# Performance work log

Hardware: AMD Instinct MI355X
Metric: run time of the kernel (lower is better)

## Reference

```python
import jax, jax.numpy as jnp
import numpy as np

H = 64
VOCAB = 64
THRESH_SCALE = 0.4
LN_EPS = 1e-5
NORM_EPS = 1e-12


def setup_inputs() -> dict:
    key = jax.random.key(0)
    ks = jax.random.split(key, 16)
    B, L = 64, 1024
    s = 1.0 / np.sqrt(H)
    inp = {
        "seq": jax.random.randint(ks[0], (B, L), 0, VOCAB),
        "embed_W": jax.random.normal(ks[1], (VOCAB, H), jnp.float32),
        "ff_W1": jax.random.normal(ks[2], (H, 2 * H), jnp.float32) * s,
        "ff_b1": jnp.zeros((2 * H,), jnp.float32),
        "ff_W2": jax.random.normal(ks[3], (2 * H, H), jnp.float32) * s,
        "ff_b2": jnp.zeros((H,), jnp.float32),
        "ln_g": jnp.ones((H,), jnp.float32),
        "ln_b": jnp.zeros((H,), jnp.float32),
        "kp_W": jax.random.normal(ks[4], (H, H), jnp.float32) * s,
        "vp_W": jax.random.normal(ks[5], (H, H), jnp.float32) * s,
        "qp_W": jax.random.normal(ks[6], (H, H), jnp.float32) * s,
        "rp_W": jax.random.normal(ks[7], (H, H), jnp.float32) * s,
        "rp_b": jnp.zeros((H,), jnp.float32),
        "out_W": jax.random.normal(ks[8], (H, VOCAB), jnp.float32) * s,
        "out_b": jnp.zeros((VOCAB,), jnp.float32),
    }
    return inp


def _forward(seq, embed_W, ff_W1, ff_b1, ff_W2, ff_b2, ln_g, ln_b,
             kp_W, vp_W, qp_W, rp_W, rp_b, out_W, out_b):
    h = embed_W[seq]                                    # [B, L, H]
    ff = jnp.maximum(h @ ff_W1 + ff_b1, 0.0) @ ff_W2 + ff_b2
    x = h + ff
    mu = x.mean(-1, keepdims=True)
    var = ((x - mu) ** 2).mean(-1, keepdims=True)       # biased var (torch LayerNorm)
    hn = (x - mu) / jnp.sqrt(var + LN_EPS) * ln_g + ln_b
    B, L, _ = hn.shape

    # Precompute all per-step keys/values, then scan the fast-weight update.
    k_all = hn[:, :-1] @ kp_W                           # [B, L-1, H]
    v_all = hn[:, :-1] @ vp_W                           # [B, L-1, H]
    kn_all = k_all / jnp.maximum(
        jnp.linalg.norm(k_all, axis=-1, keepdims=True), NORM_EPS)

    def step(M, kv):
        kn, v = kv                                      # each [B, H]
        vp = jnp.einsum('bij,bj->bi', M, kn)            # read M along k
        err = jnp.linalg.norm(v - vp, axis=-1)          # [B]
        gate = jnp.where(err > THRESH_SCALE * jnp.linalg.norm(v, axis=-1),
                         1.0, 0.0)                      # hard energy gate
        M = M + gate[:, None, None] * jnp.einsum('bi,bj->bij', v - vp, kn)
        return M, None

    M0 = jnp.zeros((B, H, H), dtype=hn.dtype)
    M, _ = jax.lax.scan(step, M0,
                        (kn_all.transpose(1, 0, 2), v_all.transpose(1, 0, 2)))

    q = hn[:, -1] @ qp_W                                # [B, H]
    r = jnp.einsum('bij,bj->bi', M, q) @ rp_W + rp_b
    return r @ out_W + out_b                            # [B, VOCAB]


def reference(seq, embed_W, ff_W1, ff_b1, ff_W2, ff_b2, ln_g, ln_b,
              kp_W, vp_W, qp_W, rp_W, rp_b, out_W, out_b):
    return _forward(seq, embed_W, ff_W1, ff_b1, ff_W2, ff_b2, ln_g, ln_b,
                    kp_W, vp_W, qp_W, rp_W, rp_b, out_W, out_b)
```

## Files before the change

### kernel.cpp

```cpp
#include <hip/hip_runtime.h>
#include <hip/hip_bf16.h>
#include <math.h>

#define BB 64
#define LL 1024
#define HH 64

typedef float v4f __attribute__((ext_vector_type(4)));

__global__ __launch_bounds__(256, 1)
void token_kernel(const int* __restrict__ seq,
                  const float* __restrict__ embed_W,
                  const float* __restrict__ ff_W1, const float* __restrict__ ff_b1,
                  const float* __restrict__ ff_W2, const float* __restrict__ ff_b2,
                  const float* __restrict__ ln_g, const float* __restrict__ ln_b,
                  const float* __restrict__ kp_W, const float* __restrict__ vp_W,
                  const float* __restrict__ qp_W,
                  float* __restrict__ knv, float* __restrict__ vthr,
                  float* __restrict__ qbuf)
{
    __shared__ __align__(16) float h_s[32][64];
    __shared__ __align__(16) float t1_s[32][128];
    __shared__ __align__(16) float hn_s[32][64];

    const int tid  = threadIdx.x;
    const int tok0 = blockIdx.x * 32;

#pragma unroll
    for (int k = 0; k < 8; ++k) {
        int e   = k * 256 + tid;
        int tok = e >> 6, i = e & 63;
        int s   = seq[tok0 + tok];
        h_s[tok][i] = embed_W[s * 64 + i];
    }
    __syncthreads();

    {
        const int j = tid & 127;
        const int g = tid >> 7;
        float w1c[64];
#pragma unroll
        for (int ii = 0; ii < 64; ++ii) w1c[ii] = ff_W1[ii * 128 + j];
        const float b1j = ff_b1[j];
#pragma unroll
        for (int tk = 0; tk < 16; ++tk) {
            const int tok = g * 16 + tk;
            const float4* h4 = (const float4*)h_s[tok];
            float a0 = b1j, a1 = 0.f, a2 = 0.f, a3 = 0.f;
#pragma unroll
            for (int w = 0; w < 16; ++w) {
                float4 hv = h4[w];
                a0 = fmaf(hv.x, w1c[4*w+0], a0);
                a1 = fmaf(hv.y, w1c[4*w+1], a1);
                a2 = fmaf(hv.z, w1c[4*w+2], a2);
                a3 = fmaf(hv.w, w1c[4*w+3], a3);
            }
            t1_s[tok][j] = fmaxf((a0 + a1) + (a2 + a3), 0.f);
        }
    }
    __syncthreads();

    {
        const int i  = tid & 63;
        const int w4 = tid >> 6;
        const float b2i = ff_b2[i];
        const float gi  = ln_g[i];
        const float bi  = ln_b[i];
        float accf[8];
#pragma unroll
        for (int tk = 0; tk < 8; ++tk) accf[tk] = b2i;
#pragma unroll
        for (int h = 0; h < 2; ++h) {
            float w2c[64];
#pragma unroll
            for (int jj = 0; jj < 64; ++jj) w2c[jj] = ff_W2[(h*64 + jj) * 64 + i];
#pragma unroll
            for (int tk = 0; tk < 8; ++tk) {
                const int tok = w4 * 8 + tk;
                const float4* t4 = (const float4*)&t1_s[tok][h*64];
                float a0 = 0.f, a1 = 0.f, a2 = 0.f, a3 = 0.f;
#pragma unroll
                for (int w = 0; w < 16; ++w) {
                    float4 tv = t4[w];
                    a0 = fmaf(tv.x, w2c[4*w+0], a0);
                    a1 = fmaf(tv.y, w2c[4*w+1], a1);
                    a2 = fmaf(tv.z, w2c[4*w+2], a2);
                    a3 = fmaf(tv.w, w2c[4*w+3], a3);
                }
                accf[tk] += (a0 + a1) + (a2 + a3);
            }
        }
#pragma unroll
        for (int tk = 0; tk < 8; ++tk) {
            const int tok = w4 * 8 + tk;
            float x = h_s[tok][i] + accf[tk];
            float s = x;
#pragma unroll
            for (int m = 32; m > 0; m >>= 1) s += __shfl_xor(s, m);
            float mu = s * (1.f / 64.f);
            float d  = x - mu;
            float s2 = d * d;
#pragma unroll
            for (int m = 32; m > 0; m >>= 1) s2 += __shfl_xor(s2, m);
            float var = s2 * (1.f / 64.f);
            hn_s[tok][i] = d / sqrtf(var + 1e-5f) * gi + bi;
        }
    }
    __syncthreads();

    {
        const int i  = tid & 63;
        const int w4 = tid >> 6;
        float kc[64], vc[64];
#pragma unroll
        for (int ii = 0; ii < 64; ++ii) {
            kc[ii] = kp_W[ii * 64 + i];
            vc[ii] = vp_W[ii * 64 + i];
        }
#pragma unroll
        for (int tk = 0; tk < 8; ++tk) {
            const int tok = w4 * 8 + tk;
            const int tg  = tok0 + tok;
            const int b   = tg >> 10;
            const int t   = tg & 1023;
            const float4* hn4 = (const float4*)hn_s[tok];
            if (t < 1023) {
                float ka0=0.f,ka1=0.f,ka2=0.f,ka3=0.f;
                float va0=0.f,va1=0.f,va2=0.f,va3=0.f;
#pragma unroll
                for (int w = 0; w < 16; ++w) {
                    float4 hv = hn4[w];
                    ka0 = fmaf(hv.x, kc[4*w+0], ka0);
                    ka1 = fmaf(hv.y, kc[4*w+1], ka1);
                    ka2 = fmaf(hv.z, kc[4*w+2], ka2);
                    ka3 = fmaf(hv.w, kc[4*w+3], ka3);
                    va0 = fmaf(hv.x, vc[4*w+0], va0);
                    va1 = fmaf(hv.y, vc[4*w+1], va1);
                    va2 = fmaf(hv.z, vc[4*w+2], va2);
                    va3 = fmaf(hv.w, vc[4*w+3], va3);
                }
                float ka = (ka0 + ka1) + (ka2 + ka3);
                float va = (va0 + va1) + (va2 + va3);
                float kn2 = ka * ka, vn2 = va * va;
#pragma unroll
                for (int m = 32; m > 0; m >>= 1) {
                    kn2 += __shfl_xor(kn2, m);
                    vn2 += __shfl_xor(vn2, m);
                }
                float knorm = fmaxf(sqrtf(kn2), 1e-12f);
                size_t row = ((size_t)b * 1024 + t) * 128;
                knv[row + i]      = ka / knorm;
                knv[row + 64 + i] = va;
                if (i == 0) vthr[b * 1024 + t] = 0.16f * vn2;
            } else {
                float qa0=0.f,qa1=0.f,qa2=0.f,qa3=0.f;
#pragma unroll
                for (int w = 0; w < 16; ++w) {
                    float4 hv = hn4[w];
                    qa0 = fmaf(hv.x, qp_W[(4*w+0)*64 + i], qa0);
                    qa1 = fmaf(hv.y, qp_W[(4*w+1)*64 + i], qa1);
                    qa2 = fmaf(hv.z, qp_W[(4*w+2)*64 + i], qa2);
                    qa3 = fmaf(hv.w, qp_W[(4*w+3)*64 + i], qa3);
                }
                qbuf[b * 64 + i] = (qa0 + qa1) + (qa2 + qa3);
            }
        }
    }
}


template<int CTRL>
__device__ __forceinline__ float dppadd(float x) {
    int y = __builtin_amdgcn_update_dpp(0, __float_as_int(x), CTRL, 0xF, 0xF, true);
    return x + __int_as_float(y);
}

__device__ __forceinline__ float wave_sum64(float x) {
    x = dppadd<0x111>(x); x = dppadd<0x112>(x);
    x = dppadd<0x114>(x); x = dppadd<0x118>(x);
    x = dppadd<0x142>(x); x = dppadd<0x143>(x);
    return __int_as_float(__builtin_amdgcn_readlane(__float_as_int(x), 63));
}

#define RPT16(F) F(0) F(1) F(2) F(3) F(4) F(5) F(6) F(7) \
                 F(8) F(9) F(10) F(11) F(12) F(13) F(14) F(15)

#define INITM(i) v4f m##i = {0.f, 0.f, 0.f, 0.f};
#define QFMA(i)  accq = __builtin_elementwise_fma(m##i, qq[i], accq);

#define LOADK16(P, NROW) do { \
    const v4f* kk_ = (const v4f*)(NROW); \
    P##0 = kk_[0];  P##1 = kk_[1];  P##2 = kk_[2];  P##3 = kk_[3]; \
    P##4 = kk_[4];  P##5 = kk_[5];  P##6 = kk_[6];  P##7 = kk_[7]; \
    P##8 = kk_[8];  P##9 = kk_[9];  P##10 = kk_[10]; P##11 = kk_[11]; \
    P##12 = kk_[12]; P##13 = kk_[13]; P##14 = kk_[14]; P##15 = kk_[15]; \
} while (0)

#define UPD16(P) do { \
    v4f gv_ = {gd_s, gd_s, gd_s, gd_s}; \
    m0  = __builtin_elementwise_fma(gv_, P##0,  m0 ); \
    m1  = __builtin_elementwise_fma(gv_, P##1,  m1 ); \
    m2  = __builtin_elementwise_fma(gv_, P##2,  m2 ); \
    m3  = __builtin_elementwise_fma(gv_, P##3,  m3 ); \
    m4  = __builtin_elementwise_fma(gv_, P##4,  m4 ); \
    m5  = __builtin_elementwise_fma(gv_, P##5,  m5 ); \
    m6  = __builtin_elementwise_fma(gv_, P##6,  m6 ); \
    m7  = __builtin_elementwise_fma(gv_, P##7,  m7 ); \
    m8  = __builtin_elementwise_fma(gv_, P##8,  m8 ); \
    m9  = __builtin_elementwise_fma(gv_, P##9,  m9 ); \
    m10 = __builtin_elementwise_fma(gv_, P##10, m10); \
    m11 = __builtin_elementwise_fma(gv_, P##11, m11); \
    m12 = __builtin_elementwise_fma(gv_, P##12, m12); \
    m13 = __builtin_elementwise_fma(gv_, P##13, m13); \
    m14 = __builtin_elementwise_fma(gv_, P##14, m14); \
    m15 = __builtin_elementwise_fma(gv_, P##15, m15); \
} while (0)

#define DOT16(P, OUT) do { \
    v4f s0_ = __builtin_elementwise_fma(m0,  P##0, \
              __builtin_elementwise_fma(m4,  P##4, \
              __builtin_elementwise_fma(m8,  P##8,  m12 * P##12))); \
    v4f s1_ = __builtin_elementwise_fma(m1,  P##1, \
              __builtin_elementwise_fma(m5,  P##5, \
              __builtin_elementwise_fma(m9,  P##9,  m13 * P##13))); \
    v4f s2_ = __builtin_elementwise_fma(m2,  P##2, \
              __builtin_elementwise_fma(m6,  P##6, \
              __builtin_elementwise_fma(m10, P##10, m14 * P##14))); \
    v4f s3_ = __builtin_elementwise_fma(m3,  P##3, \
              __builtin_elementwise_fma(m7,  P##7, \
              __builtin_elementwise_fma(m11, P##11, m15 * P##15))); \
    v4f st_ = (s0_ + s1_) + (s2_ + s3_); \
    OUT = (st_.x + st_.y) + (st_.z + st_.w); \
} while (0)

#define ITER2(X, Y, ROW2, TH2P2) do { \
    float nbase_; \
    DOT16(X, nbase_);                        \
    float knl2_ = (ROW2)[lane]; \
    float vv2_  = (ROW2)[64 + lane]; \
    float t22_  = *(TH2P2); \
    float vp_ = fmaf(c_s, gd_s, base_s);     \
    float d_  = vv_s - vp_; \
    float e_  = wave_sum64(d_ * d_); \
    gd_s = (e_ > t2_s) ? d_ : 0.0f;          \
    float cn_ = wave_sum64(knl_cur * knl_nxt);   \
    UPD16(Y);                                \
    LOADK16(Y, ROW2);                        \
    base_s = nbase_;  c_s = cn_; \
    knl_cur = knl_nxt; knl_nxt = knl2_; \
    vv_s = vv_nxt;     vv_nxt = vv2_; \
    t2_s = t2_nxt;     t2_nxt = t22_; \
} while (0)

#define CHUNK16_2(CB, NB, TP) \
    ITER2(A,B,(CB)+2*128,(TP)+2);   ITER2(B,A,(CB)+3*128,(TP)+3); \
    ITER2(A,B,(CB)+4*128,(TP)+4);   ITER2(B,A,(CB)+5*128,(TP)+5); \
    ITER2(A,B,(CB)+6*128,(TP)+6);   ITER2(B,A,(CB)+7*128,(TP)+7); \
    ITER2(A,B,(CB)+8*128,(TP)+8);   ITER2(B,A,(CB)+9*128,(TP)+9); \
    ITER2(A,B,(CB)+10*128,(TP)+10); ITER2(B,A,(CB)+11*128,(TP)+11); \
    ITER2(A,B,(CB)+12*128,(TP)+12); ITER2(B,A,(CB)+13*128,(TP)+13); \
    ITER2(A,B,(CB)+14*128,(TP)+14); ITER2(B,A,(CB)+15*128,(TP)+15); \
    ITER2(A,B,(NB)+0*128,(TP)+16);  ITER2(B,A,(NB)+1*128,(TP)+17);

#define CHUNK15_2(CB, NB, TP) \
    ITER2(A,B,(CB)+2*128,(TP)+2);   ITER2(B,A,(CB)+3*128,(TP)+3); \
    ITER2(A,B,(CB)+4*128,(TP)+4);   ITER2(B,A,(CB)+5*128,(TP)+5); \
    ITER2(A,B,(CB)+6*128,(TP)+6);   ITER2(B,A,(CB)+7*128,(TP)+7); \
    ITER2(A,B,(CB)+8*128,(TP)+8);   ITER2(B,A,(CB)+9*128,(TP)+9); \
    ITER2(A,B,(CB)+10*128,(TP)+10); ITER2(B,A,(CB)+11*128,(TP)+11); \
    ITER2(A,B,(CB)+12*128,(TP)+12); ITER2(B,A,(CB)+13*128,(TP)+13); \
    ITER2(A,B,(CB)+14*128,(TP)+14); ITER2(B,A,(CB)+15*128,(TP)+15); \
    ITER2(A,B,(NB)+0*128,(TP)+16);

__device__ __forceinline__ void gl2lds_1k(const float* g, float* l, int lane) {
    __builtin_amdgcn_global_load_lds(
        (const __attribute__((address_space(1))) void*)(g + lane * 4),
        (__attribute__((address_space(3))) void*)l, 16, 0, 0);
}

__device__ __forceinline__ void prefetch_chunk(const float* g, float* l, int lane) {
#pragma unroll
    for (int w = 0; w < 8; ++w)
        gl2lds_1k(g + w * 256, l + w * 256, lane);
}

__global__ __launch_bounds__(64, 1)
void scan_kernel(const float* __restrict__ knv,
                 const float* __restrict__ vthr,
                 const float* __restrict__ qbuf,
                 const float* __restrict__ rp_W, const float* __restrict__ rp_b,
                 const float* __restrict__ out_W, const float* __restrict__ out_b,
                 float* __restrict__ out)
{
    const int b    = blockIdx.x;
    const int lane = threadIdx.x;
    const float* knvb = knv  + (size_t)b * 1024 * 128;
    const float* thrb = vthr + (size_t)b * 1024;

    __shared__ __align__(16) float thr_s[1040];
    __shared__ __align__(16) float buf[3 * 2048];
    __shared__ float sh[64];

    RPT16(INITM)

    v4f A0,A1,A2,A3,A4,A5,A6,A7,A8,A9,A10,A11,A12,A13,A14,A15;
    v4f B0,B1,B2,B3,B4,B5,B6,B7,B8,B9,B10,B11,B12,B13,B14,B15;

#pragma unroll
    for (int w = 0; w < 4; ++w) gl2lds_1k(thrb + w * 256, thr_s + w * 256, lane);
    prefetch_chunk(knvb,        buf,        lane);
    prefetch_chunk(knvb + 2048, buf + 2048, lane);
    prefetch_chunk(knvb + 4096, buf + 4096, lane);

    asm volatile("s_waitcnt vmcnt(16)" ::: "memory");

    LOADK16(B, buf);
    LOADK16(A, buf + 128);
    float knl_cur = buf[lane];
    float knl_nxt = buf[128 + lane];
    float vv_s    = buf[64 + lane];
    float vv_nxt  = buf[192 + lane];
    float t2_s    = thr_s[0];
    float t2_nxt  = thr_s[1];
    float gd_s = 0.f, base_s = 0.f, c_s = 0.f;

#pragma unroll 1
    for (int c = 0; c < 62; ++c) {
        asm volatile("s_waitcnt vmcnt(8)" ::: "memory");
        const float* cb = buf + (c % 3) * 2048;
        const float* nb = buf + ((c + 1) % 3) * 2048;
        const float* tp = thr_s + c * 16;
        CHUNK16_2(cb, nb, tp)
        if (c <= 60)
            prefetch_chunk(knvb + (size_t)(c + 3) * 2048,
                           buf + (c % 3) * 2048, lane);
    }
    asm volatile("s_waitcnt vmcnt(0)" ::: "memory");
    {
        const float* cb = buf + 2 * 2048;
        const float* nb = buf;
        const float* tp = thr_s + 62 * 16;
        CHUNK16_2(cb, nb, tp)
    }
    {
        const float* cb = buf;
        const float* nb = buf + 2048;
        const float* tp = thr_s + 63 * 16;
        CHUNK15_2(cb, nb, tp)
    }

    const v4f* qq = (const v4f*)(qbuf + b * 64);
    v4f accq = {0.f, 0.f, 0.f, 0.f};
    RPT16(QFMA)
    float vq = (accq.x + accq.y) + (accq.z + accq.w);

    sh[lane] = vq;
    __syncthreads();
    float r = rp_b[lane];
#pragma unroll
    for (int ii = 0; ii < 64; ++ii) r = fmaf(sh[ii], rp_W[ii * 64 + lane], r);
    __syncthreads();
    sh[lane] = r;
    __syncthreads();
    float o = out_b[lane];
#pragma unroll
    for (int ii = 0; ii < 64; ++ii) o = fmaf(sh[ii], out_W[ii * 64 + lane], o);
    out[b * 64 + lane] = o;
}

extern "C" void kernel_launch(void* const* d_in, const int* in_sizes, int n_in,
                              void* d_out, int out_size, void* d_ws, size_t ws_size,
                              hipStream_t stream)
{
    const int*   seq   = (const int*)  d_in[0];
    const float* embed = (const float*)d_in[1];
    const float* ffW1  = (const float*)d_in[2];
    const float* ffb1  = (const float*)d_in[3];
    const float* ffW2  = (const float*)d_in[4];
    const float* ffb2  = (const float*)d_in[5];
    const float* lng   = (const float*)d_in[6];
    const float* lnb   = (const float*)d_in[7];
    const float* kpW   = (const float*)d_in[8];
    const float* vpW   = (const float*)d_in[9];
    const float* qpW   = (const float*)d_in[10];
    const float* rpW   = (const float*)d_in[11];
    const float* rpb   = (const float*)d_in[12];
    const float* outW  = (const float*)d_in[13];
    const float* outb  = (const float*)d_in[14];
    float* out = (float*)d_out;

    float* knv  = (float*)d_ws;
    float* vthr = knv  + (size_t)64 * 1024 * 128;
    float* qbuf = vthr + (size_t)64 * 1024;

    token_kernel<<<2048, 256, 0, stream>>>(seq, embed, ffW1, ffb1, ffW2, ffb2,
                                           lng, lnb, kpW, vpW, qpW,
                                           knv, vthr, qbuf);
    scan_kernel<<<64, 64, 0, stream>>>(knv, vthr, qbuf,
                                       rpW, rpb, outW, outb, out);
}
```

Before: 435.3 us.

## Reload key rows from LDS each step instead of double-buffering in registers

The scan loop now reloads both the current and previous key rows from shared memory every step, rather than keeping two register banks that swap roles across steps. The next base dot product is computed after the gate instead of being issued ahead of it, and the final rank-1 update is applied after the loop. This removes the A/B role alternation and may simplify register allocation, at the cost of twice the LDS reads per step and a longer dependency chain, since the dot product no longer overlaps the reductions.

```diff
diff --git a/kernel.cpp b/kernel.cpp
--- a/kernel.cpp
+++ b/kernel.cpp
@@ -233,9 +233,10 @@
     OUT = (st_.x + st_.y) + (st_.z + st_.w); \
 } while (0)
 
-#define ITER2(X, Y, ROW2, TH2P2) do { \
-    float nbase_; \
-    DOT16(X, nbase_);                        \
+#define ITER(XROW, UROW, ROW2, TH2P2) do { \
+    LOADK16(A, XROW);                        \
+    UPD16(B);                                \
+    LOADK16(B, UROW);                        \
     float knl2_ = (ROW2)[lane]; \
     float vv2_  = (ROW2)[64 + lane]; \
     float t22_  = *(TH2P2); \
@@ -244,33 +245,47 @@
     float e_  = wave_sum64(d_ * d_); \
     gd_s = (e_ > t2_s) ? d_ : 0.0f;          \
     float cn_ = wave_sum64(knl_cur * knl_nxt);   \
-    UPD16(Y);                                \
-    LOADK16(Y, ROW2);                        \
-    base_s = nbase_;  c_s = cn_; \
+    DOT16(A, base_s);                        \
+    c_s = cn_; \
     knl_cur = knl_nxt; knl_nxt = knl2_; \
     vv_s = vv_nxt;     vv_nxt = vv2_; \
     t2_s = t2_nxt;     t2_nxt = t22_; \
 } while (0)
 
-#define CHUNK16_2(CB, NB, TP) \
-    ITER2(A,B,(CB)+2*128,(TP)+2);   ITER2(B,A,(CB)+3*128,(TP)+3); \
-    ITER2(A,B,(CB)+4*128,(TP)+4);   ITER2(B,A,(CB)+5*128,(TP)+5); \
-    ITER2(A,B,(CB)+6*128,(TP)+6);   ITER2(B,A,(CB)+7*128,(TP)+7); \
-    ITER2(A,B,(CB)+8*128,(TP)+8);   ITER2(B,A,(CB)+9*128,(TP)+9); \
-    ITER2(A,B,(CB)+10*128,(TP)+10); ITER2(B,A,(CB)+11*128,(TP)+11); \
-    ITER2(A,B,(CB)+12*128,(TP)+12); ITER2(B,A,(CB)+13*128,(TP)+13); \
-    ITER2(A,B,(CB)+14*128,(TP)+14); ITER2(B,A,(CB)+15*128,(TP)+15); \
-    ITER2(A,B,(NB)+0*128,(TP)+16);  ITER2(B,A,(NB)+1*128,(TP)+17);
-
-#define CHUNK15_2(CB, NB, TP) \
-    ITER2(A,B,(CB)+2*128,(TP)+2);   ITER2(B,A,(CB)+3*128,(TP)+3); \
-    ITER2(A,B,(CB)+4*128,(TP)+4);   ITER2(B,A,(CB)+5*128,(TP)+5); \
-    ITER2(A,B,(CB)+6*128,(TP)+6);   ITER2(B,A,(CB)+7*128,(TP)+7); \
-    ITER2(A,B,(CB)+8*128,(TP)+8);   ITER2(B,A,(CB)+9*128,(TP)+9); \
-    ITER2(A,B,(CB)+10*128,(TP)+10); ITER2(B,A,(CB)+11*128,(TP)+11); \
-    ITER2(A,B,(CB)+12*128,(TP)+12); ITER2(B,A,(CB)+13*128,(TP)+13); \
-    ITER2(A,B,(CB)+14*128,(TP)+14); ITER2(B,A,(CB)+15*128,(TP)+15); \
-    ITER2(A,B,(NB)+0*128,(TP)+16);
+#define CHUNK16_D(CB, NB, TP) \
+    ITER((CB)+1*128,  (CB)+0*128,  (CB)+2*128,  (TP)+2); \
+    ITER((CB)+2*128,  (CB)+1*128,  (CB)+3*128,  (TP)+3); \
+    ITER((CB)+3*128,  (CB)+2*128,  (CB)+4*128,  (TP)+4); \
+    ITER((CB)+4*128,  (CB)+3*128,  (CB)+5*128,  (TP)+5); \
+    ITER((CB)+5*128,  (CB)+4*128,  (CB)+6*128,  (TP)+6); \
+    ITER((CB)+6*128,  (CB)+5*128,  (CB)+7*128,  (TP)+7); \
+    ITER((CB)+7*128,  (CB)+6*128,  (CB)+8*128,  (TP)+8); \
+    ITER((CB)+8*128,  (CB)+7*128,  (CB)+9*128,  (TP)+9); \
+    ITER((CB)+9*128,  (CB)+8*128,  (CB)+10*128, (TP)+10); \
+    ITER((CB)+10*128, (CB)+9*128,  (CB)+11*128, (TP)+11); \
+    ITER((CB)+11*128, (CB)+10*128, (CB)+12*128, (TP)+12); \
+    ITER((CB)+12*128, (CB)+11*128, (CB)+13*128, (TP)+13); \
+    ITER((CB)+13*128, (CB)+12*128, (CB)+14*128, (TP)+14); \
+    ITER((CB)+14*128, (CB)+13*128, (CB)+15*128, (TP)+15); \
+    ITER((CB)+15*128, (CB)+14*128, (NB)+0*128,  (TP)+16); \
+    ITER((NB)+0*128,  (CB)+15*128, (NB)+1*128,  (TP)+17);
+
+#define CHUNK15_D(CB, NB, TP) \
+    ITER((CB)+1*128,  (CB)+0*128,  (CB)+2*128,  (TP)+2); \
+    ITER((CB)+2*128,  (CB)+1*128,  (CB)+3*128,  (TP)+3); \
+    ITER((CB)+3*128,  (CB)+2*128,  (CB)+4*128,  (TP)+4); \
+    ITER((CB)+4*128,  (CB)+3*128,  (CB)+5*128,  (TP)+5); \
+    ITER((CB)+5*128,  (CB)+4*128,  (CB)+6*128,  (TP)+6); \
+    ITER((CB)+6*128,  (CB)+5*128,  (CB)+7*128,  (TP)+7); \
+    ITER((CB)+7*128,  (CB)+6*128,  (CB)+8*128,  (TP)+8); \
+    ITER((CB)+8*128,  (CB)+7*128,  (CB)+9*128,  (TP)+9); \
+    ITER((CB)+9*128,  (CB)+8*128,  (CB)+10*128, (TP)+10); \
+    ITER((CB)+10*128, (CB)+9*128,  (CB)+11*128, (TP)+11); \
+    ITER((CB)+11*128, (CB)+10*128, (CB)+12*128, (TP)+12); \
+    ITER((CB)+12*128, (CB)+11*128, (CB)+13*128, (TP)+13); \
+    ITER((CB)+13*128, (CB)+12*128, (CB)+14*128, (TP)+14); \
+    ITER((CB)+14*128, (CB)+13*128, (CB)+15*128, (TP)+15); \
+    ITER((CB)+15*128, (CB)+14*128, (NB)+0*128,  (TP)+16);
 
 __device__ __forceinline__ void gl2lds_1k(const float* g, float* l, int lane) {
     __builtin_amdgcn_global_load_lds(
@@ -314,8 +329,11 @@
 
     asm volatile("s_waitcnt vmcnt(16)" ::: "memory");
 
-    LOADK16(B, buf);
-    LOADK16(A, buf + 128);
+    {
+        v4f z_ = {0.f, 0.f, 0.f, 0.f};
+        B0=z_;B1=z_;B2=z_;B3=z_;B4=z_;B5=z_;B6=z_;B7=z_;
+        B8=z_;B9=z_;B10=z_;B11=z_;B12=z_;B13=z_;B14=z_;B15=z_;
+    }
     float knl_cur = buf[lane];
     float knl_nxt = buf[128 + lane];
     float vv_s    = buf[64 + lane];
@@ -330,7 +348,7 @@
         const float* cb = buf + (c % 3) * 2048;
         const float* nb = buf + ((c + 1) % 3) * 2048;
         const float* tp = thr_s + c * 16;
-        CHUNK16_2(cb, nb, tp)
+        CHUNK16_D(cb, nb, tp)
         if (c <= 60)
             prefetch_chunk(knvb + (size_t)(c + 3) * 2048,
                            buf + (c % 3) * 2048, lane);
@@ -340,14 +358,15 @@
         const float* cb = buf + 2 * 2048;
         const float* nb = buf;
         const float* tp = thr_s + 62 * 16;
-        CHUNK16_2(cb, nb, tp)
+        CHUNK16_D(cb, nb, tp)
     }
     {
         const float* cb = buf;
         const float* nb = buf + 2048;
         const float* tp = thr_s + 63 * 16;
-        CHUNK15_2(cb, nb, tp)
-    }
+        CHUNK15_D(cb, nb, tp)
+    }
+    UPD16(B);
 
     const v4f* qq = (const v4f*)(qbuf + b * 64);
     v4f accq = {0.f, 0.f, 0.f, 0.f};
```

Result: slower. 468.0 us (+7.5%).

## Split fast-weight matrix columns across two waves with LDS partial-sum exchange

Applied to the files above, without the earlier changes.

The scan kernel now runs two wavefronts per batch. Each wave holds half of every row of M (32 columns), so per-step register work and LDS key loads are halved. Each step the waves swap partial read-dot products through a double-buffered LDS array and meet at an s_barrier. The aim is to shorten the latency-bound serial critical path per step. The cost is a barrier plus an LDS round trip on every one of the ~1023 sequential steps.

```diff
diff --git a/kernel.cpp b/kernel.cpp
--- a/kernel.cpp
+++ b/kernel.cpp
@@ -7,6 +7,7 @@
 #define HH 64
 
 typedef float v4f __attribute__((ext_vector_type(4)));
+#define F4 __builtin_elementwise_fma
 
 __global__ __launch_bounds__(256, 1)
 void token_kernel(const int* __restrict__ seq,
@@ -182,95 +183,66 @@
     return __int_as_float(__builtin_amdgcn_readlane(__float_as_int(x), 63));
 }
 
-#define RPT16(F) F(0) F(1) F(2) F(3) F(4) F(5) F(6) F(7) \
-                 F(8) F(9) F(10) F(11) F(12) F(13) F(14) F(15)
-
-#define INITM(i) v4f m##i = {0.f, 0.f, 0.f, 0.f};
-#define QFMA(i)  accq = __builtin_elementwise_fma(m##i, qq[i], accq);
-
-#define LOADK16(P, NROW) do { \
-    const v4f* kk_ = (const v4f*)(NROW); \
-    P##0 = kk_[0];  P##1 = kk_[1];  P##2 = kk_[2];  P##3 = kk_[3]; \
-    P##4 = kk_[4];  P##5 = kk_[5];  P##6 = kk_[6];  P##7 = kk_[7]; \
-    P##8 = kk_[8];  P##9 = kk_[9];  P##10 = kk_[10]; P##11 = kk_[11]; \
-    P##12 = kk_[12]; P##13 = kk_[13]; P##14 = kk_[14]; P##15 = kk_[15]; \
+#define LOADK8(P, ROW) do { \
+    const float* rA_ = (ROW) + (wid << 3); \
+    const float* rB_ = rA_ + 4; \
+    P##A0 = *(const v4f*)(rA_ +  0); P##A1 = *(const v4f*)(rA_ + 16); \
+    P##A2 = *(const v4f*)(rA_ + 32); P##A3 = *(const v4f*)(rA_ + 48); \
+    P##B0 = *(const v4f*)(rB_ +  0); P##B1 = *(const v4f*)(rB_ + 16); \
+    P##B2 = *(const v4f*)(rB_ + 32); P##B3 = *(const v4f*)(rB_ + 48); \
 } while (0)
 
-#define UPD16(P) do { \
+#define UPD8(P) do { \
     v4f gv_ = {gd_s, gd_s, gd_s, gd_s}; \
-    m0  = __builtin_elementwise_fma(gv_, P##0,  m0 ); \
-    m1  = __builtin_elementwise_fma(gv_, P##1,  m1 ); \
-    m2  = __builtin_elementwise_fma(gv_, P##2,  m2 ); \
-    m3  = __builtin_elementwise_fma(gv_, P##3,  m3 ); \
-    m4  = __builtin_elementwise_fma(gv_, P##4,  m4 ); \
-    m5  = __builtin_elementwise_fma(gv_, P##5,  m5 ); \
-    m6  = __builtin_elementwise_fma(gv_, P##6,  m6 ); \
-    m7  = __builtin_elementwise_fma(gv_, P##7,  m7 ); \
-    m8  = __builtin_elementwise_fma(gv_, P##8,  m8 ); \
-    m9  = __builtin_elementwise_fma(gv_, P##9,  m9 ); \
-    m10 = __builtin_elementwise_fma(gv_, P##10, m10); \
-    m11 = __builtin_elementwise_fma(gv_, P##11, m11); \
-    m12 = __builtin_elementwise_fma(gv_, P##12, m12); \
-    m13 = __builtin_elementwise_fma(gv_, P##13, m13); \
-    m14 = __builtin_elementwise_fma(gv_, P##14, m14); \
-    m15 = __builtin_elementwise_fma(gv_, P##15, m15); \
+    mA0 = F4(gv_, P##A0, mA0); mA1 = F4(gv_, P##A1, mA1); \
+    mA2 = F4(gv_, P##A2, mA2); mA3 = F4(gv_, P##A3, mA3); \
+    mB0 = F4(gv_, P##B0, mB0); mB1 = F4(gv_, P##B1, mB1); \
+    mB2 = F4(gv_, P##B2, mB2); mB3 = F4(gv_, P##B3, mB3); \
 } while (0)
 
-#define DOT16(P, OUT) do { \
-    v4f s0_ = __builtin_elementwise_fma(m0,  P##0, \
-              __builtin_elementwise_fma(m4,  P##4, \
-              __builtin_elementwise_fma(m8,  P##8,  m12 * P##12))); \
-    v4f s1_ = __builtin_elementwise_fma(m1,  P##1, \
-              __builtin_elementwise_fma(m5,  P##5, \
-              __builtin_elementwise_fma(m9,  P##9,  m13 * P##13))); \
-    v4f s2_ = __builtin_elementwise_fma(m2,  P##2, \
-              __builtin_elementwise_fma(m6,  P##6, \
-              __builtin_elementwise_fma(m10, P##10, m14 * P##14))); \
-    v4f s3_ = __builtin_elementwise_fma(m3,  P##3, \
-              __builtin_elementwise_fma(m7,  P##7, \
-              __builtin_elementwise_fma(m11, P##11, m15 * P##15))); \
-    v4f st_ = (s0_ + s1_) + (s2_ + s3_); \
-    OUT = (st_.x + st_.y) + (st_.z + st_.w); \
-} while (0)
-
-#define ITER2(X, Y, ROW2, TH2P2) do { \
-    float nbase_; \
-    DOT16(X, nbase_);                        \
+#define ITER(X, Y, ROW2, TH2P2, P) do { \
+    v4f po_ = ((const v4f*)pex[P][1 - wid])[lane];       \
+    v4f sA_ = F4(mA0, X##A0, F4(mA1, X##A1, F4(mA2, X##A2, mA3 * X##A3))); \
+    v4f sB_ = F4(mB0, X##B0, F4(mB1, X##B1, F4(mB2, X##B2, mB3 * X##B3))); \
+    v4f pn_ = sA_ + sB_;                                 \
     float knl2_ = (ROW2)[lane]; \
     float vv2_  = (ROW2)[64 + lane]; \
     float t22_  = *(TH2P2); \
-    float vp_ = fmaf(c_s, gd_s, base_s);     \
+    v4f st_ = pown_prev + po_;                           \
+    float base_ = (st_.x + st_.y) + (st_.z + st_.w); \
+    float vp_ = fmaf(c_s, gd_s, base_); \
     float d_  = vv_s - vp_; \
     float e_  = wave_sum64(d_ * d_); \
-    gd_s = (e_ > t2_s) ? d_ : 0.0f;          \
-    float cn_ = wave_sum64(knl_cur * knl_nxt);   \
-    UPD16(Y);                                \
-    LOADK16(Y, ROW2);                        \
-    base_s = nbase_;  c_s = cn_; \
-    knl_cur = knl_nxt; knl_nxt = knl2_; \
-    vv_s = vv_nxt;     vv_nxt = vv2_; \
-    t2_s = t2_nxt;     t2_nxt = t22_; \
+    gd_s = (e_ > t2_s) ? d_ : 0.0f;                      \
+    float cn_ = wave_sum64(knl_cur * knl_nxt); \
+    UPD8(Y);                                             \
+    LOADK8(Y, ROW2);                                     \
+    ((v4f*)pex[(P) ^ 1][wid])[lane] = pn_;               \
+    pown_prev = pn_; \
+    c_s = cn_; knl_cur = knl_nxt; knl_nxt = knl2_; \
+    vv_s = vv_nxt; vv_nxt = vv2_; t2_s = t2_nxt; t2_nxt = t22_; \
+    asm volatile("s_waitcnt lgkmcnt(0)\n\ts_barrier" ::: "memory"); \
 } while (0)
 
-#define CHUNK16_2(CB, NB, TP) \
-    ITER2(A,B,(CB)+2*128,(TP)+2);   ITER2(B,A,(CB)+3*128,(TP)+3); \
-    ITER2(A,B,(CB)+4*128,(TP)+4);   ITER2(B,A,(CB)+5*128,(TP)+5); \
-    ITER2(A,B,(CB)+6*128,(TP)+6);   ITER2(B,A,(CB)+7*128,(TP)+7); \
-    ITER2(A,B,(CB)+8*128,(TP)+8);   ITER2(B,A,(CB)+9*128,(TP)+9); \
-    ITER2(A,B,(CB)+10*128,(TP)+10); ITER2(B,A,(CB)+11*128,(TP)+11); \
-    ITER2(A,B,(CB)+12*128,(TP)+12); ITER2(B,A,(CB)+13*128,(TP)+13); \
-    ITER2(A,B,(CB)+14*128,(TP)+14); ITER2(B,A,(CB)+15*128,(TP)+15); \
-    ITER2(A,B,(NB)+0*128,(TP)+16);  ITER2(B,A,(NB)+1*128,(TP)+17);
-
-#define CHUNK15_2(CB, NB, TP) \
-    ITER2(A,B,(CB)+2*128,(TP)+2);   ITER2(B,A,(CB)+3*128,(TP)+3); \
-    ITER2(A,B,(CB)+4*128,(TP)+4);   ITER2(B,A,(CB)+5*128,(TP)+5); \
-    ITER2(A,B,(CB)+6*128,(TP)+6);   ITER2(B,A,(CB)+7*128,(TP)+7); \
-    ITER2(A,B,(CB)+8*128,(TP)+8);   ITER2(B,A,(CB)+9*128,(TP)+9); \
-    ITER2(A,B,(CB)+10*128,(TP)+10); ITER2(B,A,(CB)+11*128,(TP)+11); \
-    ITER2(A,B,(CB)+12*128,(TP)+12); ITER2(B,A,(CB)+13*128,(TP)+13); \
-    ITER2(A,B,(CB)+14*128,(TP)+14); ITER2(B,A,(CB)+15*128,(TP)+15); \
-    ITER2(A,B,(NB)+0*128,(TP)+16);
+#define CHUNK16_W(CB, NB, TP) \
+    ITER(S,T,(CB)+2*128,(TP)+2,0);   ITER(T,S,(CB)+3*128,(TP)+3,1); \
+    ITER(S,T,(CB)+4*128,(TP)+4,0);   ITER(T,S,(CB)+5*128,(TP)+5,1); \
+    ITER(S,T,(CB)+6*128,(TP)+6,0);   ITER(T,S,(CB)+7*128,(TP)+7,1); \
+    ITER(S,T,(CB)+8*128,(TP)+8,0);   ITER(T,S,(CB)+9*128,(TP)+9,1); \
+    ITER(S,T,(CB)+10*128,(TP)+10,0); ITER(T,S,(CB)+11*128,(TP)+11,1); \
+    ITER(S,T,(CB)+12*128,(TP)+12,0); ITER(T,S,(CB)+13*128,(TP)+13,1); \
+    ITER(S,T,(CB)+14*128,(TP)+14,0); ITER(T,S,(CB)+15*128,(TP)+15,1); \
+    ITER(S,T,(NB)+0*128,(TP)+16,0);  ITER(T,S,(NB)+1*128,(TP)+17,1);
+
+#define CHUNK15_W(CB, NB, TP) \
+    ITER(S,T,(CB)+2*128,(TP)+2,0);   ITER(T,S,(CB)+3*128,(TP)+3,1); \
+    ITER(S,T,(CB)+4*128,(TP)+4,0);   ITER(T,S,(CB)+5*128,(TP)+5,1); \
+    ITER(S,T,(CB)+6*128,(TP)+6,0);   ITER(T,S,(CB)+7*128,(TP)+7,1); \
+    ITER(S,T,(CB)+8*128,(TP)+8,0);   ITER(T,S,(CB)+9*128,(TP)+9,1); \
+    ITER(S,T,(CB)+10*128,(TP)+10,0); ITER(T,S,(CB)+11*128,(TP)+11,1); \
+    ITER(S,T,(CB)+12*128,(TP)+12,0); ITER(T,S,(CB)+13*128,(TP)+13,1); \
+    ITER(S,T,(CB)+14*128,(TP)+14,0); ITER(T,S,(CB)+15*128,(TP)+15,1); \
+    ITER(S,T,(NB)+0*128,(TP)+16,0);
 
 __device__ __forceinline__ void gl2lds_1k(const float* g, float* l, int lane) {
     __builtin_amdgcn_global_load_lds(
@@ -278,13 +250,14 @@
         (__attribute__((address_space(3))) void*)l, 16, 0, 0);
 }
 
-__device__ __forceinline__ void prefetch_chunk(const float* g, float* l, int lane) {
-#pragma unroll
-    for (int w = 0; w < 8; ++w)
-        gl2lds_1k(g + w * 256, l + w * 256, lane);
-}
-
-__global__ __launch_bounds__(64, 1)
+__device__ __forceinline__ void prefetch_half(const float* g, float* l,
+                                              int lane, int wid) {
+#pragma unroll
+    for (int j = 0; j < 4; ++j)
+        gl2lds_1k(g + wid * 1024 + j * 256, l + wid * 1024 + j * 256, lane);
+}
+
+__global__ __launch_bounds__(128, 1)
 void scan_kernel(const float* __restrict__ knv,
                  const float* __restrict__ vthr,
                  const float* __restrict__ qbuf,
@@ -293,79 +266,102 @@
                  float* __restrict__ out)
 {
     const int b    = blockIdx.x;
-    const int lane = threadIdx.x;
+    const int tid  = threadIdx.x;
+    const int lane = tid & 63;
+    const int wid  = tid >> 6;
     const float* knvb = knv  + (size_t)b * 1024 * 128;
     const float* thrb = vthr + (size_t)b * 1024;
 
     __shared__ __align__(16) float thr_s[1040];
     __shared__ __align__(16) float buf[3 * 2048];
+    __shared__ __align__(16) float pex[2][2][256];
     __shared__ float sh[64];
 
-    RPT16(INITM)
-
-    v4f A0,A1,A2,A3,A4,A5,A6,A7,A8,A9,A10,A11,A12,A13,A14,A15;
-    v4f B0,B1,B2,B3,B4,B5,B6,B7,B8,B9,B10,B11,B12,B13,B14,B15;
-
-#pragma unroll
-    for (int w = 0; w < 4; ++w) gl2lds_1k(thrb + w * 256, thr_s + w * 256, lane);
-    prefetch_chunk(knvb,        buf,        lane);
-    prefetch_chunk(knvb + 2048, buf + 2048, lane);
-    prefetch_chunk(knvb + 4096, buf + 4096, lane);
-
-    asm volatile("s_waitcnt vmcnt(16)" ::: "memory");
-
-    LOADK16(B, buf);
-    LOADK16(A, buf + 128);
+    v4f mA0={0,0,0,0},mA1={0,0,0,0},mA2={0,0,0,0},mA3={0,0,0,0};
+    v4f mB0={0,0,0,0},mB1={0,0,0,0},mB2={0,0,0,0},mB3={0,0,0,0};
+    v4f SA0,SA1,SA2,SA3,SB0,SB1,SB2,SB3;
+    v4f TA0,TA1,TA2,TA3,TB0,TB1,TB2,TB3;
+
+    if (wid == 0) {
+#pragma unroll
+        for (int w = 0; w < 4; ++w) gl2lds_1k(thrb + w * 256, thr_s + w * 256, lane);
+    }
+    prefetch_half(knvb,        buf,        lane, wid);
+    prefetch_half(knvb + 2048, buf + 2048, lane, wid);
+    prefetch_half(knvb + 4096, buf + 4096, lane, wid);
+
+    {
+        v4f z_ = {0.f, 0.f, 0.f, 0.f};
+        ((v4f*)pex)[tid] = z_;
+    }
+
+    asm volatile("s_waitcnt vmcnt(4) lgkmcnt(0)\n\ts_barrier" ::: "memory");
+
+    LOADK8(T, buf);
+    LOADK8(S, buf + 128);
+    v4f pown_prev = {0.f, 0.f, 0.f, 0.f};
     float knl_cur = buf[lane];
     float knl_nxt = buf[128 + lane];
     float vv_s    = buf[64 + lane];
     float vv_nxt  = buf[192 + lane];
     float t2_s    = thr_s[0];
     float t2_nxt  = thr_s[1];
-    float gd_s = 0.f, base_s = 0.f, c_s = 0.f;
+    float gd_s = 0.f, c_s = 0.f;
 
 #pragma unroll 1
     for (int c = 0; c < 62; ++c) {
-        asm volatile("s_waitcnt vmcnt(8)" ::: "memory");
+        asm volatile("s_waitcnt vmcnt(4)" ::: "memory");
         const float* cb = buf + (c % 3) * 2048;
         const float* nb = buf + ((c + 1) % 3) * 2048;
         const float* tp = thr_s + c * 16;
-        CHUNK16_2(cb, nb, tp)
+        CHUNK16_W(cb, nb, tp)
         if (c <= 60)
-            prefetch_chunk(knvb + (size_t)(c + 3) * 2048,
-                           buf + (c % 3) * 2048, lane);
+            prefetch_half(knvb + (size_t)(c + 3) * 2048,
+                          buf + (c % 3) * 2048, lane, wid);
     }
     asm volatile("s_waitcnt vmcnt(0)" ::: "memory");
+    asm volatile("s_barrier" ::: "memory");
     {
         const float* cb = buf + 2 * 2048;
         const float* nb = buf;
         const float* tp = thr_s + 62 * 16;
-        CHUNK16_2(cb, nb, tp)
+        CHUNK16_W(cb, nb, tp)
     }
     {
         const float* cb = buf;
         const float* nb = buf + 2048;
         const float* tp = thr_s + 63 * 16;
-        CHUNK15_2(cb, nb, tp)
-    }
-
-    const v4f* qq = (const v4f*)(qbuf + b * 64);
-    v4f accq = {0.f, 0.f, 0.f, 0.f};
-    RPT16(QFMA)
-    float vq = (accq.x + accq.y) + (accq.z + accq.w);
-
-    sh[lane] = vq;
-    __syncthreads();
-    float r = rp_b[lane];
-#pragma unroll
-    for (int ii = 0; ii < 64; ++ii) r = fmaf(sh[ii], rp_W[ii * 64 + lane], r);
-    __syncthreads();
-    sh[lane] = r;
-    __syncthreads();
-    float o = out_b[lane];
-#pragma unroll
-    for (int ii = 0; ii < 64; ++ii) o = fmaf(sh[ii], out_W[ii * 64 + lane], o);
-    out[b * 64 + lane] = o;
+        CHUNK15_W(cb, nb, tp)
+    }
+
+    {
+        const v4f* qq = (const v4f*)(qbuf + b * 64);
+        const int w2 = 2 * wid;
+        v4f aqA = F4(mA0, qq[w2+0], F4(mA1, qq[w2+4],
+                  F4(mA2, qq[w2+8],  mA3 * qq[w2+12])));
+        v4f aqB = F4(mB0, qq[w2+1], F4(mB1, qq[w2+5],
+                  F4(mB2, qq[w2+9],  mB3 * qq[w2+13])));
+        v4f aq = aqA + aqB;
+        float vq_own = (aq.x + aq.y) + (aq.z + aq.w);
+        ((float*)pex)[wid * 64 + lane] = vq_own;
+        asm volatile("s_waitcnt lgkmcnt(0)\n\ts_barrier" ::: "memory");
+        float vq = vq_own + ((float*)pex)[(1 - wid) * 64 + lane];
+
+        if (wid == 0) {
+            sh[lane] = vq;
+            asm volatile("s_waitcnt lgkmcnt(0)" ::: "memory");
+            float r = rp_b[lane];
+#pragma unroll
+            for (int ii = 0; ii < 64; ++ii) r = fmaf(sh[ii], rp_W[ii * 64 + lane], r);
+            asm volatile("s_waitcnt lgkmcnt(0)" ::: "memory");
+            sh[lane] = r;
+            asm volatile("s_waitcnt lgkmcnt(0)" ::: "memory");
+            float o = out_b[lane];
+#pragma unroll
+            for (int ii = 0; ii < 64; ++ii) o = fmaf(sh[ii], out_W[ii * 64 + lane], o);
+            out[b * 64 + lane] = o;
+        }
+    }
 }
 
 extern "C" void kernel_launch(void* const* d_in, const int* in_sizes, int n_in,
@@ -396,6 +392,6 @@
     token_kernel<<<2048, 256, 0, stream>>>(seq, embed, ffW1, ffb1, ffW2, ffb2,
                                            lng, lnb, kpW, vpW, qpW,
                                            knv, vthr, qbuf);
-    scan_kernel<<<64, 64, 0, stream>>>(knv, vthr, qbuf,
-                                       rpW, rpb, outW, outb, out);
-}
+    scan_kernel<<<64, 128, 0, stream>>>(knv, vthr, qbuf,
+                                        rpW, rpb, outW, outb, out);
+}
```

New measurement: 417.0 us. 1.04x faster.
